# Performance work log

Measured on AMD Instinct MI355X. Metric: run time of the kernel, lower is better.

The kernel has to match this reference:

```python
import jax, jax.numpy as jnp
import numpy as np

N_WIRES = 8
N_LAYERS = 2


def _ry(theta):
    # torchquantum RY: [[cos(t/2), -sin(t/2)], [sin(t/2), cos(t/2)]]
    c = jnp.cos(theta / 2)
    s = jnp.sin(theta / 2)
    row0 = jnp.stack([c, -s], axis=-1)
    row1 = jnp.stack([s, c], axis=-1)
    return jnp.stack([row0, row1], axis=-2).astype(jnp.complex64)


def _rz(theta):
    # torchquantum RZ: diag(exp(-i t/2), exp(+i t/2))
    e = jnp.exp(-0.5j * theta.astype(jnp.complex64))
    z = jnp.zeros_like(e)
    row0 = jnp.stack([e, z], axis=-1)
    row1 = jnp.stack([z, jnp.conj(e)], axis=-1)
    return jnp.stack([row0, row1], axis=-2)


def _apply_1q(state, gate, w):
    # state: [bsz, 2, 2, ..., 2] (wire w at axis 1+w); gate: [2,2] or [bsz,2,2]
    s = jnp.moveaxis(state, 1 + w, -1)
    if gate.ndim == 2:
        s = jnp.einsum('ab,...b->...a', gate, s)
    else:
        s = jnp.einsum('nab,n...b->n...a', gate, s)
    return jnp.moveaxis(s, -1, 1 + w)


def _apply_cnot(state, c, t):
    # control wire c, target wire t; swap target amplitudes where control=1
    s0 = jnp.take(state, 0, axis=1 + c)
    s1 = jnp.take(state, 1, axis=1 + c)
    t_ax = 1 + t if t < c else t  # target axis shifts after removing control axis
    s1 = jnp.flip(s1, axis=t_ax)
    return jnp.stack([s0, s1], axis=1 + c)


def _forward(x_image, theta_rot, hardwts):
    bsz = x_image.shape[0]
    # F.avg_pool2d(x, 6): kernel=stride=6 on 28x28 -> 4x4 (last 4 rows/cols dropped)
    xp = x_image[..., :24, :24].reshape(bsz, 1, 4, 6, 4, 6).mean(axis=(3, 5))
    x = xp.reshape(bsz, N_WIRES, 2)

    # |0...0> state, wire w at axis 1+w (torchquantum layout)
    state = jnp.zeros((bsz, 2 ** N_WIRES), jnp.complex64).at[:, 0].set(1.0)
    state = state.reshape((bsz,) + (2,) * N_WIRES)

    k_sel = jnp.argmax(hardwts, axis=1)  # [8], one-hot row -> selected op index

    for layer in range(N_LAYERS):
        for j in range(N_WIRES):
            if layer == 0:
                # GeneralEncoder: ry(x[:,j,0]) then rz(x[:,j,1]) on wire j
                state = _apply_1q(state, _ry(x[:, j, 0]), j)
                state = _apply_1q(state, _rz(x[:, j, 1]), j)

            def rot_branch(s, layer=layer, j=j):
                th = theta_rot[layer, j]
                s = _apply_1q(s, _rz(th[0]), j)
                s = _apply_1q(s, _ry(th[1]), j)
                s = _apply_1q(s, _rz(th[2]), j)
                return s

            branches = []
            for k in range(N_WIRES + 1):
                if k == N_WIRES:
                    branches.append(rot_branch)
                elif k == j:
                    branches.append(lambda s: s)  # identity gate
                else:
                    branches.append(lambda s, j=j, k=k: _apply_cnot(s, j, k))
            state = jax.lax.switch(k_sel[j], branches, state)

    # MeasureAll(PauliZ): <Z_w> = P(bit_w=0) - P(bit_w=1)
    probs = state.real ** 2 + state.imag ** 2
    exp_val = []
    for w in range(N_WIRES):
        p = jnp.moveaxis(probs, 1 + w, 1).reshape(bsz, 2, -1).sum(axis=-1)
        exp_val.append(p[:, 0] - p[:, 1])
    exp_val = jnp.stack(exp_val, axis=1)  # [bsz, 8]
    return jax.nn.log_softmax(exp_val, axis=1)


def setup_inputs() -> dict:
    key = jax.random.key(0)
    k1, k2 = jax.random.split(key)
    bsz = 8192
    x_image = jax.random.normal(k1, (bsz, 1, 28, 28), dtype=jnp.float32)
    theta_rot = np.pi * jax.random.uniform(k2, (N_LAYERS, N_WIRES, 3), dtype=jnp.float32)
    # one-hot selection per qubit; at least one row selects k=8 (rotation block),
    # matching the torch rejection loop's acceptance condition
    sel = np.array([8, 0, 8, 5, 3, 8, 6, 8])
    hw = np.zeros((N_WIRES, N_WIRES + 1), np.int32)
    hw[np.arange(N_WIRES), sel] = 1
    return {"x_image": x_image, "theta_rot": theta_rot, "hardwts": jnp.asarray(hw)}


def reference(x_image, theta_rot, hardwts):
    return _forward(x_image, theta_rot, hardwts)
```

## Files before the change

### kernel.cpp

```cpp
#include <hip/hip_runtime.h>
#include <math.h>


__device__ __forceinline__ float bpermf(int addr_bytes, float v) {
    return __int_as_float(__builtin_amdgcn_ds_bpermute(addr_bytes, __float_as_int(v)));
}
__device__ __forceinline__ unsigned bpermu(int addr_bytes, unsigned v) {
    return (unsigned)__builtin_amdgcn_ds_bpermute(addr_bytes, (int)v);
}

template<int CTRL>
__device__ __forceinline__ float dppf(float x) {
    return __int_as_float(__builtin_amdgcn_mov_dpp(__float_as_int(x), CTRL, 0xF, 0xF, true));
}

#define NPC_PK 0x0F5AA5F0u
#define NPT_PK 0xE4B1B1E4u
#define NSG_PK 0x00000480u

__device__ __forceinline__ void bloch_gather(const float2 pv[9], int hof,
                                             float Xc[8], float Yc[8], float Zc[8]) {
    float sum = 0.f;
#pragma unroll
    for (int q = 0; q < 9; ++q) sum += pv[q].x + pv[q].y;
    sum += __shfl_xor(sum, 16, 64);
    float ang = sum * (1.0f / 36.0f);
    float s_a = __sinf(ang), c_a = __cosf(ang);
    float sbp = dppf<0xB1>(s_a);
    float cbp = dppf<0xB1>(c_a);
    float bx = s_a * cbp;
    float by = s_a * sbp;
    float bz = c_a;
#pragma unroll
    for (int j = 0; j < 8; ++j) {
        int src = hof + 2 * j;
        Xc[j] = __shfl(bx, src, 64);
        Yc[j] = __shfl(by, src, 64);
        Zc[j] = __shfl(bz, src, 64);
    }
}

__global__ __launch_bounds__(1024, 4) void qnet_one(
    const float* __restrict__ x_image,
    const float* __restrict__ theta_rot,
    const int*   __restrict__ hardwts,
    float*       __restrict__ out,
    int bsz)
{
    __shared__ __align__(16) float    tabF[8][16];
    __shared__ __align__(16) unsigned tabU[8][16];

    const int tid  = threadIdx.x;
    const int lane = tid & 63;
    const int wid  = tid >> 6;
    const int sub  = lane & 31;
    const int hb   = lane >> 5;
    const int hof  = lane & 32;
    int bidx = blockIdx.x * 32 + wid * 2 + hb;
    int bidxc = bidx < bsz ? bidx : bsz - 1;
    const float* img = x_image + (size_t)bidxc * 784;

    const int cell = sub & 15, rh4 = sub >> 4;
    const int ry = cell >> 2, rx = cell & 3;
    float2 pv[9];
#pragma unroll
    for (int rr = 0; rr < 3; ++rr) {
        const float* rp = img + (ry * 6 + rh4 * 3 + rr) * 28 + rx * 6;
#pragma unroll
        for (int cc = 0; cc < 3; ++cc)
            pv[rr * 3 + cc] = *reinterpret_cast<const float2*>(rp + 2 * cc);
    }

    float Xc[8], Yc[8], Zc[8];
    const bool builder = (wid < 4);

    if (builder) {
        int ksel[8];
#pragma unroll
        for (int j = 0; j < 8; ++j) {
            int base = j * 9;
            int best = hardwts[base], k = 0;
#pragma unroll
            for (int kk = 1; kk <= 8; ++kk) {
                int v = hardwts[base + kk];
                if (v > best) { best = v; k = kk; }
            }
            ksel[j] = k;
        }

        const int grp  = lane >> 5;
        const int obs  = (wid << 1) | grp;
        const int slot = sub;
        const int s3   = slot / 3;
        const int w3   = slot - 3 * s3;
        const int paddr = (s3 + hof) << 2;

        float    cf = (slot == 0) ? 1.f : 0.f;
        unsigned cd = (slot == 0) ? (3u << (2 * obs)) : 0u;
        int cnt = 1;

#pragma unroll 1
        for (int step = 0; step < 16; ++step) {
            const int layer = (step < 8) ? 1 : 0;
            const int j = 7 - (step & 7);
            int k = ksel[j];
            if (k == 8) {
                int pred = ((cd >> (2 * j)) & 3) != 0;
                unsigned long long bal = __ballot(pred);
                unsigned myhalf = (unsigned)(bal >> hof);
                if (myhalf != 0) {
                    float t0 = theta_rot[layer*24 + j*3 + 0];
                    float t1 = theta_rot[layer*24 + j*3 + 1];
                    float t2 = theta_rot[layer*24 + j*3 + 2];
                    float c0 = __cosf(t0), s0 = __sinf(t0);
                    float c1 = __cosf(t1), s1 = __sinf(t1);
                    float c2 = __cosf(t2), s2 = __sinf(t2);
                    float    pcf = bpermf(paddr, cf);
                    unsigned pcd = bpermu(paddr, cd);
                    int p = (pcd >> (2 * j)) & 3;
                    bool valid = (s3 < cnt);
                    float cx = (p == 1) ? 1.f : 0.f;
                    float cy = (p == 2) ? 1.f : 0.f;
                    float cz = (p == 3) ? 1.f : 0.f;
                    { float nx = cx*c2 + cy*s2, ny = cy*c2 - cx*s2; cx = nx; cy = ny; }
                    { float nx = cx*c1 - cz*s1, nz = cx*s1 + cz*c1; cx = nx; cz = nz; }
                    { float nx = cx*c0 + cy*s0, ny = cy*c0 - cx*s0; cx = nx; cy = ny; }
                    float comp = (w3 == 0) ? cx : (w3 == 1) ? cy : cz;
                    unsigned base2   = pcd & ~(3u << (2 * j));
                    unsigned ncd_rot = base2 | ((unsigned)(w3 + 1) << (2 * j));
                    float    ncf_rot = pcf * comp;
                    bool  isI  = (p == 0);
                    float    ncf0 = (w3 == 0) ? pcf : 0.f;
                    unsigned ncd0 = (w3 == 0) ? pcd : 0u;
                    cf = valid ? (isI ? ncf0 : ncf_rot) : 0.f;
                    cd = valid ? (isI ? ncd0 : ncd_rot) : 0u;
                    cnt = (3 * cnt > 32) ? 32 : 3 * cnt;
                }
            } else if (k != j) {
                int pc = (cd >> (2 * j)) & 3;
                int pt = (cd >> (2 * k)) & 3;
                int idx = pc * 4 + pt;
                unsigned npc = (NPC_PK >> (2 * idx)) & 3u;
                unsigned npt = (NPT_PK >> (2 * idx)) & 3u;
                cd = (cd & ~((3u << (2 * j)) | (3u << (2 * k))))
                     | (npc << (2 * j)) | (npt << (2 * k));
                cf = ((NSG_PK >> idx) & 1u) ? -cf : cf;
            }
        }

        if (slot < 16) { tabF[obs][slot] = cf; tabU[obs][slot] = cd; }
    } else {
        bloch_gather(pv, hof, Xc, Yc, Zc);
    }

    __syncthreads();

    if (builder) bloch_gather(pv, hof, Xc, Yc, Zc);

    const int w = (sub >> 2) & 7, ls = sub & 3;
    float4 cf4 = *reinterpret_cast<const float4*>(&tabF[w][ls * 4]);
    uint4  cd4 = *reinterpret_cast<const uint4 *>(&tabU[w][ls * 4]);
    const float    cfa[4] = { cf4.x, cf4.y, cf4.z, cf4.w };
    const unsigned cda[4] = { cd4.x, cd4.y, cd4.z, cd4.w };

    float acc = 0.f;
#pragma unroll
    for (int kslot = 0; kslot < 4; ++kslot) {
        float p = cfa[kslot];
        unsigned code = cda[kslot];
#define APPLY(J) { int s_ = (int)((code >> (2*J)) & 3u); \
    float f_ = 1.0f; f_ = (s_==1) ? Xc[J] : f_; f_ = (s_==2) ? Yc[J] : f_; \
    f_ = (s_==3) ? Zc[J] : f_;  p *= f_; }
        APPLY(0) APPLY(1) APPLY(2) APPLY(3) APPLY(4) APPLY(5) APPLY(6) APPLY(7)
#undef APPLY
        acc += p;
    }

    acc += dppf<0xB1>(acc);
    acc += dppf<0x4E>(acc);
    float ev = acc;

    float e  = __expf(ev);
    float se = e;
    se += __shfl_xor(se, 4, 64);
    se += __shfl_xor(se, 8, 64);
    se += __shfl_xor(se, 16, 64);
    float res = ev - __logf(se);

    if (ls == 0 && bidx < bsz)
        out[(size_t)bidx * 8 + w] = res;
}

extern "C" void kernel_launch(void* const* d_in, const int* in_sizes, int n_in,
                              void* d_out, int out_size, void* d_ws, size_t ws_size,
                              hipStream_t stream) {
    const float* x_image   = (const float*)d_in[0];
    const float* theta_rot = (const float*)d_in[1];
    const int*   hardwts   = (const int*)d_in[2];
    float*       out       = (float*)d_out;
    int bsz = in_sizes[0] / 784;
    hipLaunchKernelGGL(qnet_one, dim3((bsz + 31) / 32), dim3(1024), 0, stream,
                       x_image, theta_rot, hardwts, out, bsz);
}
```

Before: 11.67 us.

## Stage image rows into LDS with coalesced global_load_lds before pooling

```diff
diff --git a/kernel.cpp b/kernel.cpp
--- a/kernel.cpp
+++ b/kernel.cpp
@@ -14,31 +14,16 @@
     return __int_as_float(__builtin_amdgcn_mov_dpp(__float_as_int(x), CTRL, 0xF, 0xF, true));
 }
 
+__device__ __forceinline__ void gload_lds16(const float* g, float* l) {
+    __builtin_amdgcn_global_load_lds(
+        (const __attribute__((address_space(1))) void*)g,
+        (__attribute__((address_space(3))) void*)l,
+        16, 0, 0);
+}
+
 #define NPC_PK 0x0F5AA5F0u
 #define NPT_PK 0xE4B1B1E4u
 #define NSG_PK 0x00000480u
-
-__device__ __forceinline__ void bloch_gather(const float2 pv[9], int hof,
-                                             float Xc[8], float Yc[8], float Zc[8]) {
-    float sum = 0.f;
-#pragma unroll
-    for (int q = 0; q < 9; ++q) sum += pv[q].x + pv[q].y;
-    sum += __shfl_xor(sum, 16, 64);
-    float ang = sum * (1.0f / 36.0f);
-    float s_a = __sinf(ang), c_a = __cosf(ang);
-    float sbp = dppf<0xB1>(s_a);
-    float cbp = dppf<0xB1>(c_a);
-    float bx = s_a * cbp;
-    float by = s_a * sbp;
-    float bz = c_a;
-#pragma unroll
-    for (int j = 0; j < 8; ++j) {
-        int src = hof + 2 * j;
-        Xc[j] = __shfl(bx, src, 64);
-        Yc[j] = __shfl(by, src, 64);
-        Zc[j] = __shfl(bz, src, 64);
-    }
-}
 
 __global__ __launch_bounds__(1024, 4) void qnet_one(
     const float* __restrict__ x_image,
@@ -47,6 +32,7 @@
     float*       __restrict__ out,
     int bsz)
 {
+    __shared__ __align__(16) float    ldsimg[32 * 672];
     __shared__ __align__(16) float    tabF[8][16];
     __shared__ __align__(16) unsigned tabU[8][16];
 
@@ -56,25 +42,32 @@
     const int sub  = lane & 31;
     const int hb   = lane >> 5;
     const int hof  = lane & 32;
-    int bidx = blockIdx.x * 32 + wid * 2 + hb;
-    int bidxc = bidx < bsz ? bidx : bsz - 1;
-    const float* img = x_image + (size_t)bidxc * 784;
-
-    const int cell = sub & 15, rh4 = sub >> 4;
-    const int ry = cell >> 2, rx = cell & 3;
-    float2 pv[9];
-#pragma unroll
-    for (int rr = 0; rr < 3; ++rr) {
-        const float* rp = img + (ry * 6 + rh4 * 3 + rr) * 28 + rx * 6;
-#pragma unroll
-        for (int cc = 0; cc < 3; ++cc)
-            pv[rr * 3 + cc] = *reinterpret_cast<const float2*>(rp + 2 * cc);
-    }
-
-    float Xc[8], Yc[8], Zc[8];
-    const bool builder = (wid < 4);
-
-    if (builder) {
+    const int bidx = blockIdx.x * 32 + wid * 2 + hb;
+
+    {
+        const int base = blockIdx.x * 32;
+#pragma unroll
+        for (int k = 0; k < 5; ++k) {
+            const int g = wid + 16 * k;
+            const int s = g * 64 + lane;
+            const int i = s / 168;
+            const int j = s - i * 168;
+            int gi = base + i; if (gi >= bsz) gi = bsz - 1;
+            gload_lds16(x_image + (size_t)gi * 784 + (j << 2),
+                        &ldsimg[g << 8]);
+        }
+        if (wid >= 12) {
+            const int g = wid + 68;
+            const int s = g * 64 + lane;
+            const int i = s / 168;
+            const int j = s - i * 168;
+            int gi = base + i; if (gi >= bsz) gi = bsz - 1;
+            gload_lds16(x_image + (size_t)gi * 784 + (j << 2),
+                        &ldsimg[g << 8]);
+        }
+    }
+
+    if (wid < 4) {
         int ksel[8];
 #pragma unroll
         for (int j = 0; j < 8; ++j) {
@@ -149,13 +142,39 @@
         }
 
         if (slot < 16) { tabF[obs][slot] = cf; tabU[obs][slot] = cd; }
-    } else {
-        bloch_gather(pv, hof, Xc, Yc, Zc);
     }
 
     __syncthreads();
 
-    if (builder) bloch_gather(pv, hof, Xc, Yc, Zc);
+    const float* ip = &ldsimg[(wid * 2 + hb) * 672];
+    const int cell = sub & 15, rh4 = sub >> 4;
+    const int ry = cell >> 2, rx = cell & 3;
+    float sum = 0.f;
+#pragma unroll
+    for (int rr = 0; rr < 3; ++rr) {
+        const float* rp = ip + (ry * 6 + rh4 * 3 + rr) * 28 + rx * 6;
+#pragma unroll
+        for (int cc = 0; cc < 3; ++cc) {
+            float2 v = *reinterpret_cast<const float2*>(rp + 2 * cc);
+            sum += v.x + v.y;
+        }
+    }
+    sum += __shfl_xor(sum, 16, 64);
+    float ang = sum * (1.0f / 36.0f);
+    float s_a = __sinf(ang), c_a = __cosf(ang);
+    float sbp = dppf<0xB1>(s_a);
+    float cbp = dppf<0xB1>(c_a);
+    float bx = s_a * cbp;
+    float by = s_a * sbp;
+    float bz = c_a;
+    float Xc[8], Yc[8], Zc[8];
+#pragma unroll
+    for (int j = 0; j < 8; ++j) {
+        int src = hof + 2 * j;
+        Xc[j] = __shfl(bx, src, 64);
+        Yc[j] = __shfl(by, src, 64);
+        Zc[j] = __shfl(bz, src, 64);
+    }
 
     const int w = (sub >> 2) & 7, ls = sub & 3;
     float4 cf4 = *reinterpret_cast<const float4*>(&tabF[w][ls * 4]);
```

Measured after the change: 12.26 us. 1.05x slower.
